# Kernel tuning notes

Hardware: AMD Instinct MI355X
Metric: run time of the kernel (lower is better)

The kernel has to match this reference:

```python
import jax, jax.numpy as jnp
import numpy as np

NUM_HEADS = 4
OUT_DIM = 64
IN_DIM = 128

def setup_inputs() -> dict:
    key = jax.random.key(0)
    k1, k2, k3, k4 = jax.random.split(key, 4)
    h = jax.random.normal(k1, (4, 256, IN_DIM), dtype=jnp.float32)
    adj = jax.random.randint(k2, (4, 256, 256), 0, 2).astype(jnp.int32)
    W = jax.random.normal(k3, (IN_DIM, NUM_HEADS * OUT_DIM), dtype=jnp.float32) * (1.0 / np.sqrt(IN_DIM))
    a = jax.random.normal(k4, (2 * OUT_DIM, 1), dtype=jnp.float32) * 0.1
    return {"h": h, "adj": adj, "W": W, "a": a}

def reference(h, adj, W, a):
    B, N, _ = h.shape
    H, D = NUM_HEADS, OUT_DIM
    Wh = (h @ W).reshape(B, N, H, D)                      # [B,N,H,D]
    # Exact replication of the torch repeat/view construction (row-major, same as torch.view)
    a1 = jnp.tile(Wh, (1, 1, 1, N)).reshape(B, N * H, N, D)
    a2 = jnp.tile(Wh, (1, N, 1, 1)).reshape(B, N * H, N, D)
    a_input = jnp.concatenate([a1, a2], axis=3)           # [B,N*H,N,2D]
    e = jax.nn.leaky_relu((a_input @ a)[..., 0], negative_slope=0.2)
    e = e.reshape(B, H, N, N)
    mask = adj[:, None, :, :] == 0                        # broadcast over heads
    attention = jax.nn.softmax(jnp.where(mask, -jnp.inf, e), axis=3)  # [B,H,N,N]
    h_prime = jnp.einsum('bhij,bjhd->bihd', attention, Wh)             # [B,N,H,D]
    return h_prime.reshape(B, N, H * D)
```

## Files before the change

### kernel.cpp

```cpp
#include <hip/hip_runtime.h>


typedef __attribute__((ext_vector_type(8))) short bf16x8;
typedef __attribute__((ext_vector_type(4))) float f32x4;

__device__ __forceinline__ short bf1(float x) {
  unsigned u = __builtin_bit_cast(unsigned, x);
  u = (u + 0x7FFFu + ((u >> 16) & 1u)) >> 16;
  return (short)u;
}
__device__ __forceinline__ bf16x8 pack8(float4 a, float4 b) {
  bf16x8 r;
  r[0]=bf1(a.x); r[1]=bf1(a.y); r[2]=bf1(a.z); r[3]=bf1(a.w);
  r[4]=bf1(b.x); r[5]=bf1(b.y); r[6]=bf1(b.z); r[7]=bf1(b.w);
  return r;
}

__global__ __launch_bounds__(256) void gat_fused(
    const float* __restrict__ h, const float* __restrict__ W,
    const float* __restrict__ a, const int* __restrict__ adj,
    float* __restrict__ out)
{
  const int tid  = threadIdx.x;
  const int lane = tid & 63;
  const int quad = lane >> 4;
  const int col  = lane & 15;
  const int wv   = tid >> 6;
  const int blk  = blockIdx.x;
  const int it = blk & 15, hp = (blk >> 4) & 3, b = blk >> 6;
  const int i0 = it * 16;

  __shared__ short WaTb[16][136];
  __shared__ float f2s[1024];
  __shared__ float f1v[16];
  __shared__ float att[16][260];
  __shared__ float Ps[16][132];
  __shared__ float sinv[16];

  {
    const int k = tid >> 1, pair = tid & 1;
    const float4* w4 = (const float4*)(W + k * 256 + pair * 128);
    const float4* a1 = (const float4*)a;
    const float4* a2 = (const float4*)(a + 64);
    float t0=0.f, t1=0.f, s0=0.f, s1=0.f;
#pragma unroll
    for (int d4 = 0; d4 < 16; d4++) {
      float4 x = w4[d4]; float4 u = a1[d4]; float4 v = a2[d4];
      t0 += x.x*u.x + x.y*u.y + x.z*u.z + x.w*u.w;
      s0 += x.x*v.x + x.y*v.y + x.z*v.z + x.w*v.w;
    }
#pragma unroll
    for (int d4 = 0; d4 < 16; d4++) {
      float4 x = w4[16 + d4]; float4 u = a1[d4]; float4 v = a2[d4];
      t1 += x.x*u.x + x.y*u.y + x.z*u.z + x.w*u.w;
      s1 += x.x*v.x + x.y*v.y + x.z*v.z + x.w*v.w;
    }
    WaTb[pair*2 + 0][k] = bf1(t0);
    WaTb[pair*2 + 1][k] = bf1(t1);
    WaTb[4 + pair*2 + 0][k] = bf1(s0);
    WaTb[4 + pair*2 + 1][k] = bf1(s1);
    int* zp = (int*)&WaTb[8][0];
    for (int t = tid; t < 544; t += 256) zp[t] = 0;
  }
  __syncthreads();

  {
    bf16x8 bw[4];
#pragma unroll
    for (int kk = 0; kk < 4; kk++)
      bw[kk] = *(const bf16x8*)&WaTb[col][kk*32 + quad*8];
    const int mtstar = hp*4 + (it >> 2), qstar = it & 3;
#pragma unroll
    for (int q = 0; q < 4; q++) {
      const int mt = wv*4 + q, n0 = mt*16;
      const float* hrow = h + (b*256 + n0 + col)*128 + quad*8;
      f32x4 acc = {0.f, 0.f, 0.f, 0.f};
#pragma unroll
      for (int kk = 0; kk < 4; kk++) {
        float4 lo = *(const float4*)(hrow + kk*32);
        float4 hi = *(const float4*)(hrow + kk*32 + 4);
        acc = __builtin_amdgcn_mfma_f32_16x16x32_bf16(pack8(lo, hi), bw[kk], acc, 0, 0, 0);
      }
      if (col >= 4 && col < 8) {
#pragma unroll
        for (int r = 0; r < 4; r++) f2s[(n0 + quad*4 + r)*4 + (col - 4)] = acc[r];
      }
      if (mt == mtstar && col < 4 && quad == qstar) {
#pragma unroll
        for (int r = 0; r < 4; r++) f1v[r*4 + col] = acc[r];
      }
    }
  }
  __syncthreads();

#pragma unroll
  for (int rq = 0; rq < 4; rq++) {
    const int rr = wv*4 + rq;
    const int i  = i0 + rr;
    const float s1v = f1v[rr];
    const float* f2row = f2s + (i & 3)*256;
    const int* adjrow = adj + (b*256 + i)*256;
    float e[4];
    float m = -1e30f;
#pragma unroll
    for (int jq = 0; jq < 4; jq++) {
      int j = lane + jq*64;
      float ev = s1v + f2row[j];
      ev = ev > 0.f ? ev : 0.2f * ev;
      ev = adjrow[j] ? ev : -1e30f;
      e[jq] = ev;
      m = fmaxf(m, ev);
    }
#pragma unroll
    for (int off = 32; off > 0; off >>= 1) m = fmaxf(m, __shfl_xor(m, off, 64));
    float s = 0.f;
#pragma unroll
    for (int jq = 0; jq < 4; jq++) {
      float ex = __expf(e[jq] - m);
      s += ex;
      att[rr][lane + jq*64] = ex;
    }
#pragma unroll
    for (int off = 32; off > 0; off >>= 1) s += __shfl_xor(s, off, 64);
    if (lane == 0) sinv[rr] = 1.f / s;
  }
  __syncthreads();

  {
    bf16x8 af[8];
    const float* arow = &att[col][quad*8];
#pragma unroll
    for (int kk = 0; kk < 8; kk++)
      af[kk] = pack8(*(const float4*)(arow + kk*32),
                     *(const float4*)(arow + kk*32 + 4));
#pragma unroll
    for (int nt = 0; nt < 2; nt++) {
      const int ncol = wv*32 + nt*16 + col;
      const float* hcol = h + b*32768 + ncol + quad*8*128;
      f32x4 acc = {0.f, 0.f, 0.f, 0.f};
#pragma unroll
      for (int kk = 0; kk < 8; kk++) {
        const float* hq = hcol + kk*32*128;
        float4 lo = { hq[0],       hq[128],     hq[256],     hq[384] };
        float4 hi = { hq[512],     hq[640],     hq[768],     hq[896] };
        acc = __builtin_amdgcn_mfma_f32_16x16x32_bf16(af[kk], pack8(lo, hi), acc, 0, 0, 0);
      }
#pragma unroll
      for (int r = 0; r < 4; r++) Ps[quad*4 + r][wv*32 + nt*16 + col] = acc[r];
    }
  }
  __syncthreads();

  {
    const int i = tid & 15, dq = tid >> 4;
    const float4* w4 = (const float4*)W;
    float4 acc = {0.f, 0.f, 0.f, 0.f};
    for (int k4 = 0; k4 < 32; k4++) {
      const int k = k4*4;
      float4 p  = *(const float4*)&Ps[i][k];
      float4 w0 = w4[(k+0)*64 + hp*16 + dq];
      float4 w1 = w4[(k+1)*64 + hp*16 + dq];
      float4 w2 = w4[(k+2)*64 + hp*16 + dq];
      float4 w3 = w4[(k+3)*64 + hp*16 + dq];
      acc.x += p.x*w0.x + p.y*w1.x + p.z*w2.x + p.w*w3.x;
      acc.y += p.x*w0.y + p.y*w1.y + p.z*w2.y + p.w*w3.y;
      acc.z += p.x*w0.z + p.y*w1.z + p.z*w2.z + p.w*w3.z;
      acc.w += p.x*w0.w + p.y*w1.w + p.z*w2.w + p.w*w3.w;
    }
    const float sv = sinv[i];
    float4 res = { acc.x*sv, acc.y*sv, acc.z*sv, acc.w*sv };
    *(float4*)&out[(b*256 + i0 + i)*256 + hp*64 + dq*4] = res;
  }
}

extern "C" void kernel_launch(void* const* d_in, const int* in_sizes, int n_in,
                              void* d_out, int out_size, void* d_ws, size_t ws_size,
                              hipStream_t stream) {
  const float* h   = (const float*)d_in[0];
  const int*   adj = (const int*)d_in[1];
  const float* W   = (const float*)d_in[2];
  const float* a   = (const float*)d_in[3];
  float* out = (float*)d_out;

  gat_fused<<<256, 256, 0, stream>>>(h, W, a, adj, out);
}
```

Measured before the change: 78.68 us.

## Double block threads, prefetch adj, store attention as bf16, MFMA final projection

Blocks grow from 256 to 512 threads, so each wave handles fewer rows and tiles. Adjacency rows are prefetched as int4 at kernel start to hide global latency behind the setup. Attention weights are stored in shared memory as bf16, which removes the repack before the MFMA. The final P·W projection now runs on bf16 MFMA using a transposed W slice staged in LDS instead of scalar fp32 FMAs, which adds extra W staging work and bf16 rounding error.

```diff
diff --git a/kernel.cpp b/kernel.cpp
--- a/kernel.cpp
+++ b/kernel.cpp
@@ -16,7 +16,7 @@
   return r;
 }
 
-__global__ __launch_bounds__(256) void gat_fused(
+__global__ __launch_bounds__(512) void gat_fused(
     const float* __restrict__ h, const float* __restrict__ W,
     const float* __restrict__ a, const int* __restrict__ adj,
     float* __restrict__ out)
@@ -31,36 +31,53 @@
   const int i0 = it * 16;
 
   __shared__ short WaTb[16][136];
+  __shared__ short WbT[64][136];
   __shared__ float f2s[1024];
   __shared__ float f1v[16];
-  __shared__ float att[16][260];
+  __shared__ short attb[16][264];
   __shared__ float Ps[16][132];
   __shared__ float sinv[16];
 
+  int4 adjv[2];
+#pragma unroll
+  for (int rq = 0; rq < 2; rq++) {
+    const int i = i0 + wv * 2 + rq;
+    adjv[rq] = *(const int4*)(adj + (b * 256 + i) * 256 + lane * 4);
+  }
+
   {
-    const int k = tid >> 1, pair = tid & 1;
-    const float4* w4 = (const float4*)(W + k * 256 + pair * 128);
-    const float4* a1 = (const float4*)a;
-    const float4* a2 = (const float4*)(a + 64);
-    float t0=0.f, t1=0.f, s0=0.f, s1=0.f;
+    const int k = tid & 127, part = tid >> 7;
+    const int sel = part >> 1, pair = part & 1;
+    const float4* wrow = (const float4*)(W + k * 256 + pair * 128);
+    const float4* ah = (const float4*)(a + sel * 64);
+    float s0 = 0.f, s1 = 0.f;
 #pragma unroll
     for (int d4 = 0; d4 < 16; d4++) {
-      float4 x = w4[d4]; float4 u = a1[d4]; float4 v = a2[d4];
-      t0 += x.x*u.x + x.y*u.y + x.z*u.z + x.w*u.w;
-      s0 += x.x*v.x + x.y*v.y + x.z*v.z + x.w*v.w;
+      float4 x = wrow[d4]; float4 va = ah[d4];
+      s0 += x.x*va.x + x.y*va.y + x.z*va.z + x.w*va.w;
     }
 #pragma unroll
     for (int d4 = 0; d4 < 16; d4++) {
-      float4 x = w4[16 + d4]; float4 u = a1[d4]; float4 v = a2[d4];
-      t1 += x.x*u.x + x.y*u.y + x.z*u.z + x.w*u.w;
-      s1 += x.x*v.x + x.y*v.y + x.z*v.z + x.w*v.w;
+      float4 x = wrow[16 + d4]; float4 va = ah[d4];
+      s1 += x.x*va.x + x.y*va.y + x.z*va.z + x.w*va.w;
     }
-    WaTb[pair*2 + 0][k] = bf1(t0);
-    WaTb[pair*2 + 1][k] = bf1(t1);
-    WaTb[4 + pair*2 + 0][k] = bf1(s0);
-    WaTb[4 + pair*2 + 1][k] = bf1(s1);
+    const int row0 = sel * 4 + pair * 2;
+    WaTb[row0 + 0][k] = bf1(s0);
+    WaTb[row0 + 1][k] = bf1(s1);
     int* zp = (int*)&WaTb[8][0];
-    for (int t = tid; t < 544; t += 256) zp[t] = 0;
+    for (int t = tid; t < 544; t += 512) zp[t] = 0;
+  }
+  {
+#pragma unroll
+    for (int q = 0; q < 4; q++) {
+      const int idx = q * 512 + tid;
+      const int k = idx >> 4, c4 = idx & 15;
+      float4 w4 = *(const float4*)(W + k * 256 + hp * 64 + c4 * 4);
+      WbT[c4*4 + 0][k] = bf1(w4.x);
+      WbT[c4*4 + 1][k] = bf1(w4.y);
+      WbT[c4*4 + 2][k] = bf1(w4.z);
+      WbT[c4*4 + 3][k] = bf1(w4.w);
+    }
   }
   __syncthreads();
 
@@ -71,8 +88,8 @@
       bw[kk] = *(const bf16x8*)&WaTb[col][kk*32 + quad*8];
     const int mtstar = hp*4 + (it >> 2), qstar = it & 3;
 #pragma unroll
-    for (int q = 0; q < 4; q++) {
-      const int mt = wv*4 + q, n0 = mt*16;
+    for (int q = 0; q < 2; q++) {
+      const int mt = wv*2 + q, n0 = mt*16;
       const float* hrow = h + (b*256 + n0 + col)*128 + quad*8;
       f32x4 acc = {0.f, 0.f, 0.f, 0.f};
 #pragma unroll
@@ -94,32 +111,27 @@
   __syncthreads();
 
 #pragma unroll
-  for (int rq = 0; rq < 4; rq++) {
-    const int rr = wv*4 + rq;
+  for (int rq = 0; rq < 2; rq++) {
+    const int rr = wv*2 + rq;
     const int i  = i0 + rr;
     const float s1v = f1v[rr];
-    const float* f2row = f2s + (i & 3)*256;
-    const int* adjrow = adj + (b*256 + i)*256;
-    float e[4];
-    float m = -1e30f;
-#pragma unroll
-    for (int jq = 0; jq < 4; jq++) {
-      int j = lane + jq*64;
-      float ev = s1v + f2row[j];
-      ev = ev > 0.f ? ev : 0.2f * ev;
-      ev = adjrow[j] ? ev : -1e30f;
-      e[jq] = ev;
-      m = fmaxf(m, ev);
-    }
+    float4 f2v = *(const float4*)(f2s + (i & 3)*256 + lane*4);
+    const int4 av = adjv[rq];
+    float e0 = s1v + f2v.x, e1 = s1v + f2v.y, e2 = s1v + f2v.z, e3 = s1v + f2v.w;
+    e0 = e0 > 0.f ? e0 : 0.2f*e0;  e1 = e1 > 0.f ? e1 : 0.2f*e1;
+    e2 = e2 > 0.f ? e2 : 0.2f*e2;  e3 = e3 > 0.f ? e3 : 0.2f*e3;
+    e0 = av.x ? e0 : -1e30f;  e1 = av.y ? e1 : -1e30f;
+    e2 = av.z ? e2 : -1e30f;  e3 = av.w ? e3 : -1e30f;
+    float m = fmaxf(fmaxf(e0, e1), fmaxf(e2, e3));
 #pragma unroll
     for (int off = 32; off > 0; off >>= 1) m = fmaxf(m, __shfl_xor(m, off, 64));
-    float s = 0.f;
-#pragma unroll
-    for (int jq = 0; jq < 4; jq++) {
-      float ex = __expf(e[jq] - m);
-      s += ex;
-      att[rr][lane + jq*64] = ex;
-    }
+    float x0 = __expf(e0 - m), x1 = __expf(e1 - m);
+    float x2 = __expf(e2 - m), x3 = __expf(e3 - m);
+    float s = (x0 + x1) + (x2 + x3);
+    float4 xa = {x0, x1, x2, x3};
+    float4 xb = {0.f, 0.f, 0.f, 0.f};
+    bf16x8 pk = pack8(xa, xb);
+    *(int2*)&attb[rr][lane*4] = *(int2*)&pk;
 #pragma unroll
     for (int off = 32; off > 0; off >>= 1) s += __shfl_xor(s, off, 64);
     if (lane == 0) sinv[rr] = 1.f / s;
@@ -128,48 +140,37 @@
 
   {
     bf16x8 af[8];
-    const float* arow = &att[col][quad*8];
 #pragma unroll
     for (int kk = 0; kk < 8; kk++)
-      af[kk] = pack8(*(const float4*)(arow + kk*32),
-                     *(const float4*)(arow + kk*32 + 4));
+      af[kk] = *(const bf16x8*)&attb[col][kk*32 + quad*8];
+    const float* hcol = h + b*32768 + (wv*16 + col) + quad*8*128;
+    f32x4 acc = {0.f, 0.f, 0.f, 0.f};
 #pragma unroll
-    for (int nt = 0; nt < 2; nt++) {
-      const int ncol = wv*32 + nt*16 + col;
-      const float* hcol = h + b*32768 + ncol + quad*8*128;
-      f32x4 acc = {0.f, 0.f, 0.f, 0.f};
+    for (int kk = 0; kk < 8; kk++) {
+      const float* hq = hcol + kk*32*128;
+      float4 lo = { hq[0],   hq[128], hq[256], hq[384] };
+      float4 hi = { hq[512], hq[640], hq[768], hq[896] };
+      acc = __builtin_amdgcn_mfma_f32_16x16x32_bf16(af[kk], pack8(lo, hi), acc, 0, 0, 0);
+    }
 #pragma unroll
-      for (int kk = 0; kk < 8; kk++) {
-        const float* hq = hcol + kk*32*128;
-        float4 lo = { hq[0],       hq[128],     hq[256],     hq[384] };
-        float4 hi = { hq[512],     hq[640],     hq[768],     hq[896] };
-        acc = __builtin_amdgcn_mfma_f32_16x16x32_bf16(af[kk], pack8(lo, hi), acc, 0, 0, 0);
-      }
-#pragma unroll
-      for (int r = 0; r < 4; r++) Ps[quad*4 + r][wv*32 + nt*16 + col] = acc[r];
-    }
+    for (int r = 0; r < 4; r++) Ps[quad*4 + r][wv*16 + col] = acc[r];
   }
   __syncthreads();
 
-  {
-    const int i = tid & 15, dq = tid >> 4;
-    const float4* w4 = (const float4*)W;
-    float4 acc = {0.f, 0.f, 0.f, 0.f};
-    for (int k4 = 0; k4 < 32; k4++) {
-      const int k = k4*4;
-      float4 p  = *(const float4*)&Ps[i][k];
-      float4 w0 = w4[(k+0)*64 + hp*16 + dq];
-      float4 w1 = w4[(k+1)*64 + hp*16 + dq];
-      float4 w2 = w4[(k+2)*64 + hp*16 + dq];
-      float4 w3 = w4[(k+3)*64 + hp*16 + dq];
-      acc.x += p.x*w0.x + p.y*w1.x + p.z*w2.x + p.w*w3.x;
-      acc.y += p.x*w0.y + p.y*w1.y + p.z*w2.y + p.w*w3.y;
-      acc.z += p.x*w0.z + p.y*w1.z + p.z*w2.z + p.w*w3.z;
-      acc.w += p.x*w0.w + p.y*w1.w + p.z*w2.w + p.w*w3.w;
+  if (wv < 4) {
+    f32x4 acc = {0.f, 0.f, 0.f, 0.f};
+#pragma unroll
+    for (int kk = 0; kk < 4; kk++) {
+      float4 lo = *(const float4*)&Ps[col][kk*32 + quad*8];
+      float4 hi = *(const float4*)&Ps[col][kk*32 + quad*8 + 4];
+      bf16x8 bp = *(const bf16x8*)&WbT[wv*16 + col][kk*32 + quad*8];
+      acc = __builtin_amdgcn_mfma_f32_16x16x32_bf16(pack8(lo, hi), bp, acc, 0, 0, 0);
     }
-    const float sv = sinv[i];
-    float4 res = { acc.x*sv, acc.y*sv, acc.z*sv, acc.w*sv };
-    *(float4*)&out[(b*256 + i0 + i)*256 + hp*64 + dq*4] = res;
+#pragma unroll
+    for (int r = 0; r < 4; r++) {
+      const int m = quad*4 + r;
+      out[(b*256 + i0 + m)*256 + hp*64 + wv*16 + col] = acc[r] * sinv[m];
+    }
   }
 }
 
@@ -182,5 +183,5 @@
   const float* a   = (const float*)d_in[3];
   float* out = (float*)d_out;
 
-  gat_fused<<<256, 256, 0, stream>>>(h, W, a, adj, out);
+  gat_fused<<<256, 512, 0, stream>>>(h, W, a, adj, out);
 }
```

Measured after the change: 75.99 us. -3.4%, faster.
